# Kernel optimization log

Hardware: AMD Instinct MI355X
Metric: run time of the kernel (lower is better)

## Reference

```python
import jax, jax.numpy as jnp
import numpy as np

NUM_CLASSES = 10
N = 4194304  # 2**22 samples


def setup_inputs() -> dict:
    key = jax.random.key(0)
    k1, k2 = jax.random.split(key)
    outputs = jax.random.uniform(k1, (N, NUM_CLASSES), dtype=jnp.float32)
    target = jax.random.randint(k2, (N,), 0, NUM_CLASSES, dtype=jnp.int64)
    return {"outputs": outputs, "target": target}


def reference(outputs, target):
    # y = one-hot(target) with 10 classes, float
    y = jax.nn.one_hot(target, NUM_CLASSES, dtype=outputs.dtype)  # [N, 10]
    # sum_j (outputs @ y.T)[i, j] == outputs[i] . sum_j y[j]
    # identical math to torch.sum(torch.mm(outputs, y.t()), dim=1) without the [N, N] intermediate
    col_counts = jnp.sum(y, axis=0)                 # [10] class counts
    nominator = outputs @ col_counts                # [N]
    denominator = jnp.linalg.norm(outputs) * jnp.linalg.norm(y)  # Frobenius norms
    return jnp.mean(-jnp.log(nominator / denominator))
```

## Files before the change

kernel.cpp:

```cpp
#include <hip/hip_runtime.h>
#include <math.h>

#define NUM_CLASSES 10
#define A_BLOCKS 512
#define B_BLOCKS 2048


__global__ void __launch_bounds__(256) hist_kernel(const int* __restrict__ target,
                                                   unsigned int* __restrict__ pc, int n) {
    unsigned int cnt[NUM_CLASSES];
#pragma unroll
    for (int c = 0; c < NUM_CLASSES; ++c) cnt[c] = 0u;

    const int tid = blockIdx.x * blockDim.x + threadIdx.x;
    const int stride = gridDim.x * blockDim.x;
    const int4* __restrict__ t4 = (const int4*)target;
    const int n4 = n >> 2;

    for (int i = tid; i < n4; i += stride) {
        int4 v = t4[i];
#pragma unroll
        for (int c = 0; c < NUM_CLASSES; ++c) {
            cnt[c] += (unsigned int)(v.x == c) + (unsigned int)(v.y == c) +
                      (unsigned int)(v.z == c) + (unsigned int)(v.w == c);
        }
    }

#pragma unroll
    for (int c = 0; c < NUM_CLASSES; ++c) {
        unsigned int v = cnt[c];
        for (int off = 32; off > 0; off >>= 1)
            v += (unsigned int)__shfl_down((int)v, off, 64);
        cnt[c] = v;
    }

    __shared__ unsigned int sh[4][NUM_CLASSES];
    const int wave = threadIdx.x >> 6;
    if ((threadIdx.x & 63) == 0) {
#pragma unroll
        for (int c = 0; c < NUM_CLASSES; ++c) sh[wave][c] = cnt[c];
    }
    __syncthreads();
    if (threadIdx.x < NUM_CLASSES) {
        const int c = threadIdx.x;
        pc[blockIdx.x * NUM_CLASSES + c] = sh[0][c] + sh[1][c] + sh[2][c] + sh[3][c];
    }
}

__device__ __forceinline__ void process_pair(const float4* __restrict__ o4, size_t p,
                                             const float w[NUM_CLASSES],
                                             float& sum_log, float& sumsq) {
    const float4* base = o4 + p * 5;
    float4 a = base[0];
    float4 b = base[1];
    float4 c4 = base[2];
    float4 d = base[3];
    float4 e = base[4];
    float r0[NUM_CLASSES] = {a.x, a.y, a.z, a.w, b.x, b.y, b.z, b.w, c4.x, c4.y};
    float r1[NUM_CLASSES] = {c4.z, c4.w, d.x, d.y, d.z, d.w, e.x, e.y, e.z, e.w};
    float nom0 = 0.f, nom1 = 0.f;
#pragma unroll
    for (int c = 0; c < NUM_CLASSES; ++c) {
        nom0 += r0[c] * w[c];
        nom1 += r1[c] * w[c];
        sumsq += r0[c] * r0[c] + r1[c] * r1[c];
    }
    sum_log += __logf(nom0) + __logf(nom1);
}

__global__ void __launch_bounds__(256) main_kernel(const float* __restrict__ outputs,
                                                   const unsigned int* __restrict__ pc,
                                                   float2* __restrict__ pacc, int n) {
    const int wave = threadIdx.x >> 6;
    const int lane = threadIdx.x & 63;

    unsigned int pw[NUM_CLASSES];
#pragma unroll
    for (int c = 0; c < NUM_CLASSES; ++c) pw[c] = 0u;
#pragma unroll
    for (int r = 0; r < A_BLOCKS / 256; ++r) {
        const unsigned int* row = pc + (threadIdx.x + r * 256) * NUM_CLASSES;
#pragma unroll
        for (int c = 0; c < NUM_CLASSES; ++c) pw[c] += row[c];
    }
#pragma unroll
    for (int c = 0; c < NUM_CLASSES; ++c) {
        unsigned int v = pw[c];
        for (int off = 32; off > 0; off >>= 1)
            v += (unsigned int)__shfl_down((int)v, off, 64);
        pw[c] = v;
    }
    __shared__ unsigned int shw[4][NUM_CLASSES];
    __shared__ float fw[NUM_CLASSES];
    if (lane == 0) {
#pragma unroll
        for (int c = 0; c < NUM_CLASSES; ++c) shw[wave][c] = pw[c];
    }
    __syncthreads();
    if (threadIdx.x < NUM_CLASSES) {
        const int c = threadIdx.x;
        fw[c] = (float)(shw[0][c] + shw[1][c] + shw[2][c] + shw[3][c]);
    }
    __syncthreads();
    float w[NUM_CLASSES];
#pragma unroll
    for (int c = 0; c < NUM_CLASSES; ++c) w[c] = fw[c];

    const float4* __restrict__ o4 = (const float4*)outputs;
    const int npairs = n >> 1;
    const int stride = gridDim.x * blockDim.x;
    const int tid = blockIdx.x * blockDim.x + threadIdx.x;

    float sum_log = 0.f, sumsq = 0.f;
    for (int p = tid; p < npairs; p += 2 * stride) {
        process_pair(o4, (size_t)p, w, sum_log, sumsq);
        const int p2 = p + stride;
        if (p2 < npairs) process_pair(o4, (size_t)p2, w, sum_log, sumsq);
    }

    for (int off = 32; off > 0; off >>= 1) {
        sum_log += __shfl_down(sum_log, off, 64);
        sumsq += __shfl_down(sumsq, off, 64);
    }
    __shared__ float s1[4], s2[4];
    if (lane == 0) { s1[wave] = sum_log; s2[wave] = sumsq; }
    __syncthreads();
    if (threadIdx.x == 0) {
        pacc[blockIdx.x] = make_float2(s1[0] + s1[1] + s1[2] + s1[3],
                                       s2[0] + s2[1] + s2[2] + s2[3]);
    }
}

__global__ void __launch_bounds__(256) finalize_kernel(const float2* __restrict__ pacc,
                                                       float* __restrict__ out, float fn) {
    float sum_log = 0.f, sumsq = 0.f;
    for (int i = threadIdx.x; i < B_BLOCKS; i += 256) {
        float2 v = pacc[i];
        sum_log += v.x;
        sumsq += v.y;
    }
    for (int off = 32; off > 0; off >>= 1) {
        sum_log += __shfl_down(sum_log, off, 64);
        sumsq += __shfl_down(sumsq, off, 64);
    }
    __shared__ float s1[4], s2[4];
    const int wave = threadIdx.x >> 6;
    if ((threadIdx.x & 63) == 0) { s1[wave] = sum_log; s2[wave] = sumsq; }
    __syncthreads();
    if (threadIdx.x == 0) {
        float t1 = s1[0] + s1[1] + s1[2] + s1[3];
        float t2 = s2[0] + s2[1] + s2[2] + s2[3];
        out[0] = 0.5f * logf(t2) + 0.5f * logf(fn) - t1 / fn;
    }
}

extern "C" void kernel_launch(void* const* d_in, const int* in_sizes, int n_in,
                              void* d_out, int out_size, void* d_ws, size_t ws_size,
                              hipStream_t stream) {
    const float* outputs = (const float*)d_in[0];
    const int* target = (const int*)d_in[1];
    const int n = in_sizes[1];

    unsigned int* pc = (unsigned int*)d_ws;
    float2* pacc = (float2*)((char*)d_ws + 20480);

    hist_kernel<<<A_BLOCKS, 256, 0, stream>>>(target, pc, n);
    main_kernel<<<B_BLOCKS, 256, 0, stream>>>(outputs, pc, pacc, n);
    finalize_kernel<<<1, 256, 0, stream>>>(pacc, (float*)d_out, (float)n);
}
```

Baseline: 248.1 us.

## Stage output rows through swizzled LDS and pack histogram counts into bitfields

The main kernel now has each wave load a 64-pair tile with fully coalesced float4 loads. It scatters the tile into a per-wave LDS buffer using an XOR swizzle, then reads back each lane's own 20 floats for the dot product and sum of squares. This replaces the previous strided 80-byte-per-lane access pattern. The histogram kernel accumulates class counts as 6-bit fields in one 64-bit integer and unpacks them every 8 iterations, replacing 40 compares per int4. The cost is extra LDS traffic and a scalar tail path for leftover pairs.

```diff
diff --git a/kernel.cpp b/kernel.cpp
--- a/kernel.cpp
+++ b/kernel.cpp
@@ -17,14 +17,23 @@
     const int4* __restrict__ t4 = (const int4*)target;
     const int n4 = n >> 2;
 
+    unsigned long long acc = 0ull;
+    int pend = 0;
     for (int i = tid; i < n4; i += stride) {
         int4 v = t4[i];
-#pragma unroll
-        for (int c = 0; c < NUM_CLASSES; ++c) {
-            cnt[c] += (unsigned int)(v.x == c) + (unsigned int)(v.y == c) +
-                      (unsigned int)(v.z == c) + (unsigned int)(v.w == c);
+        acc += (1ull << (6 * v.x)) + (1ull << (6 * v.y)) +
+               (1ull << (6 * v.z)) + (1ull << (6 * v.w));
+        if (++pend == 8) {
+#pragma unroll
+            for (int c = 0; c < NUM_CLASSES; ++c)
+                cnt[c] += (unsigned int)((acc >> (6 * c)) & 63ull);
+            acc = 0ull;
+            pend = 0;
         }
     }
+#pragma unroll
+    for (int c = 0; c < NUM_CLASSES; ++c)
+        cnt[c] += (unsigned int)((acc >> (6 * c)) & 63ull);
 
 #pragma unroll
     for (int c = 0; c < NUM_CLASSES; ++c) {
@@ -47,17 +56,12 @@
     }
 }
 
-__device__ __forceinline__ void process_pair(const float4* __restrict__ o4, size_t p,
-                                             const float w[NUM_CLASSES],
+__device__ __forceinline__ void compute_pair(const float4 r[5], const float w[NUM_CLASSES],
                                              float& sum_log, float& sumsq) {
-    const float4* base = o4 + p * 5;
-    float4 a = base[0];
-    float4 b = base[1];
-    float4 c4 = base[2];
-    float4 d = base[3];
-    float4 e = base[4];
-    float r0[NUM_CLASSES] = {a.x, a.y, a.z, a.w, b.x, b.y, b.z, b.w, c4.x, c4.y};
-    float r1[NUM_CLASSES] = {c4.z, c4.w, d.x, d.y, d.z, d.w, e.x, e.y, e.z, e.w};
+    float r0[NUM_CLASSES] = {r[0].x, r[0].y, r[0].z, r[0].w,
+                             r[1].x, r[1].y, r[1].z, r[1].w, r[2].x, r[2].y};
+    float r1[NUM_CLASSES] = {r[2].z, r[2].w, r[3].x, r[3].y,
+                             r[3].z, r[3].w, r[4].x, r[4].y, r[4].z, r[4].w};
     float nom0 = 0.f, nom1 = 0.f;
 #pragma unroll
     for (int c = 0; c < NUM_CLASSES; ++c) {
@@ -66,6 +70,14 @@
         sumsq += r0[c] * r0[c] + r1[c] * r1[c];
     }
     sum_log += __logf(nom0) + __logf(nom1);
+}
+
+__device__ __forceinline__ void process_pair_direct(const float4* __restrict__ o4, size_t p,
+                                                    const float w[NUM_CLASSES],
+                                                    float& sum_log, float& sumsq) {
+    const float4* base = o4 + p * 5;
+    float4 r[5] = {base[0], base[1], base[2], base[3], base[4]};
+    compute_pair(r, w, sum_log, sumsq);
 }
 
 __global__ void __launch_bounds__(256) main_kernel(const float* __restrict__ outputs,
@@ -106,17 +118,43 @@
 #pragma unroll
     for (int c = 0; c < NUM_CLASSES; ++c) w[c] = fw[c];
 
+    __shared__ float4 stage[4][5 * 64];
+    float4* my = stage[wave];
+
+    int wslot[5], rslot[5];
+#pragma unroll
+    for (int k = 0; k < 5; ++k) {
+        const int j = k * 64 + lane;
+        const int c = j % 5;
+        const int p = j / 5;
+        wslot[k] = c * 64 + (p ^ c);
+        rslot[k] = k * 64 + (lane ^ k);
+    }
+
     const float4* __restrict__ o4 = (const float4*)outputs;
     const int npairs = n >> 1;
-    const int stride = gridDim.x * blockDim.x;
+    const int ntiles = npairs >> 6;
+    const int gw = blockIdx.x * 4 + wave;
+    const int nwaves = gridDim.x * 4;
+
+    float sum_log = 0.f, sumsq = 0.f;
+    for (int tile = gw; tile < ntiles; tile += nwaves) {
+        const float4* src = o4 + (size_t)tile * 320;
+        float4 g[5];
+#pragma unroll
+        for (int k = 0; k < 5; ++k) g[k] = src[k * 64 + lane];
+#pragma unroll
+        for (int k = 0; k < 5; ++k) my[wslot[k]] = g[k];
+        float4 r[5];
+#pragma unroll
+        for (int k = 0; k < 5; ++k) r[k] = my[rslot[k]];
+        compute_pair(r, w, sum_log, sumsq);
+    }
+
+    const int done = ntiles << 6;
     const int tid = blockIdx.x * blockDim.x + threadIdx.x;
-
-    float sum_log = 0.f, sumsq = 0.f;
-    for (int p = tid; p < npairs; p += 2 * stride) {
-        process_pair(o4, (size_t)p, w, sum_log, sumsq);
-        const int p2 = p + stride;
-        if (p2 < npairs) process_pair(o4, (size_t)p2, w, sum_log, sumsq);
-    }
+    for (int p = done + tid; p < npairs; p += gridDim.x * blockDim.x)
+        process_pair_direct(o4, (size_t)p, w, sum_log, sumsq);
 
     for (int off = 32; off > 0; off >>= 1) {
         sum_log += __shfl_down(sum_log, off, 64);
```

New measurement: 248.7 us. About the same (+0.3%).

## Fuse finalize into main kernel via last-block ticket, pack histogram counts

Applied to the files above, without the earlier changes.

Removes the separate finalize launch by having the last main_kernel block, chosen with an atomic ticket, do the final reduction. The ticket is reset in hist_kernel. The histogram now packs class counts into 6-bit fields of a 64-bit accumulator and flushes every 8 int4 loads, replacing the 40 compares per load. Output loads switch to nontemporal builtins to avoid cache pollution. The cost is an extra atomic and fence per block.

```diff
diff --git a/kernel.cpp b/kernel.cpp
--- a/kernel.cpp
+++ b/kernel.cpp
@@ -5,9 +5,14 @@
 #define A_BLOCKS 512
 #define B_BLOCKS 2048
 
+typedef __attribute__((ext_vector_type(4))) float f32x4;
+
 
 __global__ void __launch_bounds__(256) hist_kernel(const int* __restrict__ target,
-                                                   unsigned int* __restrict__ pc, int n) {
+                                                   unsigned int* __restrict__ pc,
+                                                   unsigned int* __restrict__ ticket, int n) {
+    if (blockIdx.x == 0 && threadIdx.x == 0) *ticket = 0u;
+
     unsigned int cnt[NUM_CLASSES];
 #pragma unroll
     for (int c = 0; c < NUM_CLASSES; ++c) cnt[c] = 0u;
@@ -17,14 +22,23 @@
     const int4* __restrict__ t4 = (const int4*)target;
     const int n4 = n >> 2;
 
+    unsigned long long acc = 0ull;
+    int pend = 0;
     for (int i = tid; i < n4; i += stride) {
         int4 v = t4[i];
+        acc += (1ull << (6 * v.x)) + (1ull << (6 * v.y)) +
+               (1ull << (6 * v.z)) + (1ull << (6 * v.w));
+        if (++pend == 8) {
 #pragma unroll
-        for (int c = 0; c < NUM_CLASSES; ++c) {
-            cnt[c] += (unsigned int)(v.x == c) + (unsigned int)(v.y == c) +
-                      (unsigned int)(v.z == c) + (unsigned int)(v.w == c);
+            for (int c = 0; c < NUM_CLASSES; ++c)
+                cnt[c] += (unsigned int)((acc >> (6 * c)) & 63ull);
+            acc = 0ull;
+            pend = 0;
         }
     }
+#pragma unroll
+    for (int c = 0; c < NUM_CLASSES; ++c)
+        cnt[c] += (unsigned int)((acc >> (6 * c)) & 63ull);
 
 #pragma unroll
     for (int c = 0; c < NUM_CLASSES; ++c) {
@@ -47,15 +61,15 @@
     }
 }
 
-__device__ __forceinline__ void process_pair(const float4* __restrict__ o4, size_t p,
+__device__ __forceinline__ void process_pair(const f32x4* __restrict__ o4, size_t p,
                                              const float w[NUM_CLASSES],
                                              float& sum_log, float& sumsq) {
-    const float4* base = o4 + p * 5;
-    float4 a = base[0];
-    float4 b = base[1];
-    float4 c4 = base[2];
-    float4 d = base[3];
-    float4 e = base[4];
+    const f32x4* base = o4 + p * 5;
+    f32x4 a = __builtin_nontemporal_load(base + 0);
+    f32x4 b = __builtin_nontemporal_load(base + 1);
+    f32x4 c4 = __builtin_nontemporal_load(base + 2);
+    f32x4 d = __builtin_nontemporal_load(base + 3);
+    f32x4 e = __builtin_nontemporal_load(base + 4);
     float r0[NUM_CLASSES] = {a.x, a.y, a.z, a.w, b.x, b.y, b.z, b.w, c4.x, c4.y};
     float r1[NUM_CLASSES] = {c4.z, c4.w, d.x, d.y, d.z, d.w, e.x, e.y, e.z, e.w};
     float nom0 = 0.f, nom1 = 0.f;
@@ -70,7 +84,9 @@
 
 __global__ void __launch_bounds__(256) main_kernel(const float* __restrict__ outputs,
                                                    const unsigned int* __restrict__ pc,
-                                                   float2* __restrict__ pacc, int n) {
+                                                   float2* __restrict__ pacc,
+                                                   unsigned int* __restrict__ ticket,
+                                                   float* __restrict__ out, int n) {
     const int wave = threadIdx.x >> 6;
     const int lane = threadIdx.x & 63;
 
@@ -106,7 +122,7 @@
 #pragma unroll
     for (int c = 0; c < NUM_CLASSES; ++c) w[c] = fw[c];
 
-    const float4* __restrict__ o4 = (const float4*)outputs;
+    const f32x4* __restrict__ o4 = (const f32x4*)outputs;
     const int npairs = n >> 1;
     const int stride = gridDim.x * blockDim.x;
     const int tid = blockIdx.x * blockDim.x + threadIdx.x;
@@ -123,34 +139,38 @@
         sumsq += __shfl_down(sumsq, off, 64);
     }
     __shared__ float s1[4], s2[4];
+    __shared__ int is_last;
     if (lane == 0) { s1[wave] = sum_log; s2[wave] = sumsq; }
     __syncthreads();
     if (threadIdx.x == 0) {
         pacc[blockIdx.x] = make_float2(s1[0] + s1[1] + s1[2] + s1[3],
                                        s2[0] + s2[1] + s2[2] + s2[3]);
+        __threadfence();
+        unsigned int old = atomicAdd(ticket, 1u);
+        is_last = (old == (unsigned int)(gridDim.x - 1)) ? 1 : 0;
     }
-}
+    __syncthreads();
 
-__global__ void __launch_bounds__(256) finalize_kernel(const float2* __restrict__ pacc,
-                                                       float* __restrict__ out, float fn) {
-    float sum_log = 0.f, sumsq = 0.f;
-    for (int i = threadIdx.x; i < B_BLOCKS; i += 256) {
-        float2 v = pacc[i];
-        sum_log += v.x;
-        sumsq += v.y;
-    }
-    for (int off = 32; off > 0; off >>= 1) {
-        sum_log += __shfl_down(sum_log, off, 64);
-        sumsq += __shfl_down(sumsq, off, 64);
-    }
-    __shared__ float s1[4], s2[4];
-    const int wave = threadIdx.x >> 6;
-    if ((threadIdx.x & 63) == 0) { s1[wave] = sum_log; s2[wave] = sumsq; }
-    __syncthreads();
-    if (threadIdx.x == 0) {
-        float t1 = s1[0] + s1[1] + s1[2] + s1[3];
-        float t2 = s2[0] + s2[1] + s2[2] + s2[3];
-        out[0] = 0.5f * logf(t2) + 0.5f * logf(fn) - t1 / fn;
+    if (is_last) {
+        __threadfence();
+        const volatile float* pv = (const volatile float*)pacc;
+        float t1 = 0.f, t2 = 0.f;
+        for (int i = threadIdx.x; i < B_BLOCKS; i += 256) {
+            t1 += pv[2 * i];
+            t2 += pv[2 * i + 1];
+        }
+        for (int off = 32; off > 0; off >>= 1) {
+            t1 += __shfl_down(t1, off, 64);
+            t2 += __shfl_down(t2, off, 64);
+        }
+        if (lane == 0) { s1[wave] = t1; s2[wave] = t2; }
+        __syncthreads();
+        if (threadIdx.x == 0) {
+            const float fn = (float)n;
+            float a = s1[0] + s1[1] + s1[2] + s1[3];
+            float b = s2[0] + s2[1] + s2[2] + s2[3];
+            out[0] = 0.5f * logf(b) + 0.5f * logf(fn) - a / fn;
+        }
     }
 }
 
@@ -163,8 +183,8 @@
 
     unsigned int* pc = (unsigned int*)d_ws;
     float2* pacc = (float2*)((char*)d_ws + 20480);
+    unsigned int* ticket = (unsigned int*)((char*)d_ws + 36864);
 
-    hist_kernel<<<A_BLOCKS, 256, 0, stream>>>(target, pc, n);
-    main_kernel<<<B_BLOCKS, 256, 0, stream>>>(outputs, pc, pacc, n);
-    finalize_kernel<<<1, 256, 0, stream>>>(pacc, (float*)d_out, (float)n);
+    hist_kernel<<<A_BLOCKS, 256, 0, stream>>>(target, pc, ticket, n);
+    main_kernel<<<B_BLOCKS, 256, 0, stream>>>(outputs, pc, pacc, ticket, (float*)d_out, n);
 }
```

After: 358.6 us. 44.5% more time.
